# Kernel optimization log

Measured on AMD Instinct MI355X. Metric: run time of the kernel, lower is better.

Reference implementation:

```python
import jax, jax.numpy as jnp
import numpy as np

B, P, D, H, DH = 2, 2048, 1024, 16, 64
EPS = 1e-5

def layernorm(x, g, b):
    mu = jnp.mean(x, axis=-1, keepdims=True)
    var = jnp.mean((x - mu) ** 2, axis=-1, keepdims=True)
    return (x - mu) * jax.lax.rsqrt(var + EPS) * g + b

def setup_inputs() -> dict:
    key = jax.random.key(0)
    ks = jax.random.split(key, 16)
    s = lambda *sh: 1.0 / np.sqrt(sh[-2] if len(sh) > 1 else sh[-1])
    return {
        "x": jax.random.normal(ks[0], (B, P, D), jnp.float32),
        "Wq": jax.random.normal(ks[1], (H, D, DH), jnp.float32) / np.sqrt(D),
        "Wk": jax.random.normal(ks[2], (H, D, DH), jnp.float32) / np.sqrt(D),
        "Wv": jax.random.normal(ks[3], (H, D, DH), jnp.float32) / np.sqrt(D),
        "Wp": jax.random.normal(ks[4], (D, D), jnp.float32) / np.sqrt(D),
        "bp": jax.random.normal(ks[5], (D,), jnp.float32) * 0.01,
        "W1": jax.random.normal(ks[6], (D, 4 * D), jnp.float32) / np.sqrt(D),
        "b1": jax.random.normal(ks[7], (4 * D,), jnp.float32) * 0.01,
        "W2": jax.random.normal(ks[8], (4 * D, D), jnp.float32) / np.sqrt(4 * D),
        "b2": jax.random.normal(ks[9], (D,), jnp.float32) * 0.01,
        "g1": jnp.ones((D,), jnp.float32),
        "be1": jnp.zeros((D,), jnp.float32),
        "g2": jnp.ones((D,), jnp.float32),
        "be2": jnp.zeros((D,), jnp.float32),
    }

def reference(x, Wq, Wk, Wv, Wp, bp, W1, b1, W2, b2, g1, be1, g2, be2):
    Bb, Pp, Dd = x.shape
    h = layernorm(x, g1, be1)
    # per-head projections, stacked: [B,H,P,DH]
    q = jnp.einsum('bpd,hde->bhpe', h, Wq)
    k = jnp.einsum('bpd,hde->bhpe', h, Wk)
    v = jnp.einsum('bpd,hde->bhpe', h, Wv)
    # NOTE: source scales by dim_embd**-0.5 (C = x.shape[-1]), not dim_head
    scores = jnp.einsum('bhpe,bhqe->bhpq', q, k) * (Dd ** -0.5)
    mask = jnp.tril(jnp.ones((Pp, Pp), bool))
    scores = jnp.where(mask, scores, -jnp.inf)
    att = jax.nn.softmax(scores, axis=-1)
    o = jnp.einsum('bhpq,bhqe->bhpe', att, v)
    # concat heads: [B,P,H*DH]
    o = o.transpose(0, 2, 1, 3).reshape(Bb, Pp, -1)
    x = x + o @ Wp + bp
    h2 = layernorm(x, g2, be2)
    m = jax.nn.gelu(h2 @ W1 + b1, approximate=False)
    x = x + m @ W2 + b2
    return x
```

## Files before the change

### kernel.cpp

```cpp
#include <hip/hip_runtime.h>
#include <hip/hip_bf16.h>
#include <stdint.h>

typedef unsigned short u16;
typedef __attribute__((ext_vector_type(4))) float f32x4;
typedef __attribute__((ext_vector_type(8))) short bf16x8;
typedef __attribute__((ext_vector_type(4))) short bf16x4;
typedef __attribute__((ext_vector_type(4))) unsigned short u16x4;

static __device__ __forceinline__ u16 f2bf(float f) {
    union { float f; unsigned u; } v; v.f = f;
    unsigned r = v.u + 0x7fffu + ((v.u >> 16) & 1u);
    return (u16)(r >> 16);
}

static __device__ __forceinline__ void gload_lds16(const u16* g, u16* l) {
    __builtin_amdgcn_global_load_lds(
        (const __attribute__((address_space(1))) void*)(uintptr_t)g,
        (__attribute__((address_space(3))) void*)(uint32_t)(uintptr_t)l,
        16, 0, 0);
}

__global__ __launch_bounds__(256) void transpose_cast_b(
    const float* __restrict__ W, u16* __restrict__ out,
    int K, int N, long in_bs, long out_bs)
{
    __shared__ float tile[32][33];
    const float* Wb = W + (size_t)blockIdx.z * in_bs;
    u16* ob = out + (size_t)blockIdx.z * out_bs;
    int nt = blockIdx.x * 32, kt = blockIdx.y * 32;
    int tx = threadIdx.x & 31, ty = threadIdx.x >> 5;
    #pragma unroll
    for (int i = ty; i < 32; i += 8)
        tile[i][tx] = Wb[(size_t)(kt + i) * N + nt + tx];
    __syncthreads();
    #pragma unroll
    for (int i = ty; i < 32; i += 8)
        ob[(size_t)(nt + i) * K + kt + tx] = f2bf(tile[tx][i]);
}

__global__ __launch_bounds__(256) void ln_kernel(
    const float* __restrict__ x, const float* __restrict__ g,
    const float* __restrict__ be, u16* __restrict__ out)
{
    int row = blockIdx.x;
    int t = threadIdx.x;
    const float4* xr = (const float4*)(x + (size_t)row * 1024);
    float4 v = xr[t];
    float s = v.x + v.y + v.z + v.w;
    float sq = v.x * v.x + v.y * v.y + v.z * v.z + v.w * v.w;
    #pragma unroll
    for (int o = 1; o < 64; o <<= 1) {
        s  += __shfl_xor(s, o);
        sq += __shfl_xor(sq, o);
    }
    __shared__ float ps[4], pq[4];
    if ((t & 63) == 0) { ps[t >> 6] = s; pq[t >> 6] = sq; }
    __syncthreads();
    float S = ps[0] + ps[1] + ps[2] + ps[3];
    float Q = pq[0] + pq[1] + pq[2] + pq[3];
    float mu = S * (1.0f / 1024.0f);
    float var = Q * (1.0f / 1024.0f) - mu * mu;
    float rs = rsqrtf(var + 1e-5f);
    const float4 g4  = ((const float4*)g)[t];
    const float4 be4 = ((const float4*)be)[t];
    u16x4 o4;
    o4[0] = f2bf((v.x - mu) * rs * g4.x + be4.x);
    o4[1] = f2bf((v.y - mu) * rs * g4.y + be4.y);
    o4[2] = f2bf((v.z - mu) * rs * g4.z + be4.z);
    o4[3] = f2bf((v.w - mu) * rs * g4.w + be4.w);
    *(u16x4*)(out + (size_t)row * 1024 + t * 4) = o4;
}

template<int EPI>
__global__ __launch_bounds__(256) void gemm_bt(
    const u16* __restrict__ A, const u16* __restrict__ Bt,
    int M, int N, int K,
    const float* __restrict__ bias,
    void* __restrict__ Cout, u16* __restrict__ Kf, u16* __restrict__ Vf)
{
    __shared__ __align__(16) u16 SH[32768];
    const int tm = blockIdx.y * 128, tn = blockIdx.x * 128;
    const int t = threadIdx.x;
    const int lane = t & 63, wave = t >> 6;
    const int wr = wave >> 1, wc = wave & 1;
    const int lq = lane & 15, lg = lane >> 4;
    f32x4 acc[4][4] = {};

    const int srow8 = lane >> 3;
    const int skoff = ((lane & 7) ^ srow8) * 8;
    const u16* ag = A  + (size_t)(tm + wave * 32 + srow8) * K + skoff;
    const u16* bg = Bt + (size_t)(tn + wave * 32 + srow8) * K + skoff;

    auto STAGE = [&](int buf, int k0) {
        u16* ab = SH + buf * 16384 + wave * 2048;
        u16* bb = SH + buf * 16384 + 8192 + wave * 2048;
        #pragma unroll
        for (int j = 0; j < 4; ++j) {
            gload_lds16(ag + (size_t)(j * 8) * K + k0, ab + j * 512);
            gload_lds16(bg + (size_t)(j * 8) * K + k0, bb + j * 512);
        }
    };

    const int KT = K >> 6;
    STAGE(0, 0);
    STAGE(1, 64);
    asm volatile("s_waitcnt vmcnt(8)" ::: "memory");
    __builtin_amdgcn_sched_barrier(0);
    __builtin_amdgcn_s_barrier();

    for (int kt = 0; kt < KT; ++kt) {
        const int buf = kt & 1;
        const u16* abuf = SH + buf * 16384;
        const u16* bbuf = abuf + 8192;
        bf16x8 af[4][2], bfv[4][2];
        #pragma unroll
        for (int m = 0; m < 4; ++m) {
            const int row = wr * 64 + m * 16 + lq;
            #pragma unroll
            for (int kk = 0; kk < 2; ++kk) {
                const int slot = (kk * 4 + lg) ^ (row & 7);
                af[m][kk] = *(const bf16x8*)(abuf + row * 64 + slot * 8);
            }
        }
        #pragma unroll
        for (int n = 0; n < 4; ++n) {
            const int col = wc * 64 + n * 16 + lq;
            #pragma unroll
            for (int kk = 0; kk < 2; ++kk) {
                const int slot = (kk * 4 + lg) ^ (col & 7);
                bfv[n][kk] = *(const bf16x8*)(bbuf + col * 64 + slot * 8);
            }
        }
        asm volatile("s_waitcnt lgkmcnt(0)" ::: "memory");
        __builtin_amdgcn_sched_barrier(0);
        __builtin_amdgcn_s_barrier();

        const bool pre = (kt + 2 < KT);
        if (pre) STAGE(buf, (kt + 2) << 6);

        __builtin_amdgcn_s_setprio(1);
        #pragma unroll
        for (int m = 0; m < 4; ++m)
            #pragma unroll
            for (int n = 0; n < 4; ++n)
                #pragma unroll
                for (int kk = 0; kk < 2; ++kk)
                    acc[m][n] = __builtin_amdgcn_mfma_f32_16x16x32_bf16(
                        af[m][kk], bfv[n][kk], acc[m][n], 0, 0, 0);
        __builtin_amdgcn_s_setprio(0);

        if (kt + 1 < KT) {
            if (pre) asm volatile("s_waitcnt vmcnt(8)" ::: "memory");
            else     asm volatile("s_waitcnt vmcnt(0)" ::: "memory");
            __builtin_amdgcn_sched_barrier(0);
            __builtin_amdgcn_s_barrier();
        }
    }

    if (EPI == 2 || (EPI == 3 && tn < 1024)) {
        __syncthreads();
        #pragma unroll
        for (int n = 0; n < 4; ++n) {
            const int cl = wc * 64 + n * 16 + lq;
            #pragma unroll
            for (int m = 0; m < 4; ++m) {
                const int rl = wr * 64 + m * 16 + lg * 4;
                #pragma unroll
                for (int r = 0; r < 4; ++r) {
                    float v = acc[m][n][r];
                    if (EPI == 2) {
                        float xx = v + bias[tn + cl];
                        v = 0.5f * xx * (1.0f + erff(xx * 0.70710678118654752f));
                    }
                    SH[(rl + r) * 136 + cl] = f2bf(v);
                }
            }
        }
        __syncthreads();
        const int row = t >> 1, half = t & 1;
        const int ncols = (EPI == 2) ? N : 1024;
        const uint4* srow4 = (const uint4*)(SH + row * 136 + half * 64);
        uint4* drow = (uint4*)((u16*)Cout + (size_t)(tm + row) * ncols + tn + half * 64);
        #pragma unroll
        for (int i = 0; i < 8; ++i)
            drow[i] = srow4[i];
    } else if (EPI == 3) {
        __syncthreads();
        const bool isK = (tn < 2048);
        #pragma unroll
        for (int n = 0; n < 4; ++n) {
            const int cl = wc * 64 + n * 16 + lq;
            const int d = cl & 63, hl = cl >> 6;
            #pragma unroll
            for (int m = 0; m < 4; ++m) {
                const int rl0 = wr * 64 + m * 16 + lg * 4;
                #pragma unroll
                for (int r = 0; r < 4; ++r) {
                    const int rl = rl0 + r;
                    const int p = rl & 63, kl = rl >> 6;
                    int off;
                    if (isK)
                        off = ((p >> 4) * 2 + (d >> 5)) * 512 + ((d >> 3) & 3) * 128
                            + (p & 15) * 8 + (d & 7);
                    else
                        off = ((p >> 4) * 4 + (d >> 4)) * 256 + ((p >> 2) & 3) * 64
                            + (d & 15) * 4 + (p & 3);
                    SH[(hl * 2 + kl) * 4096 + off] = f2bf(acc[m][n][r]);
                }
            }
        }
        __syncthreads();
        const int img = t >> 6, ln = t & 63;
        const int hl = img >> 1, kl = img & 1;
        const int hh = ((tn - (isK ? 1024 : 2048)) >> 6) + hl;
        const int bb = tm >> 11, pp = tm & 2047;
        u16* base = (isK ? Kf : Vf) + (size_t)(bb * 16 + hh) * 131072
                  + (size_t)((pp >> 6) + kl) * 4096;
        const u16* simg = SH + img * 4096;
        #pragma unroll
        for (int i = 0; i < 8; ++i)
            *(uint4*)(base + ln * 8 + i * 512) = *(const uint4*)(simg + ln * 8 + i * 512);
    }
}

__global__ __launch_bounds__(256) void gemm_bt64(
    const u16* __restrict__ A, const u16* __restrict__ Bt,
    int M, int N, int K,
    const float* __restrict__ bias, const float* __restrict__ res,
    float* __restrict__ Cout)
{
    __shared__ __align__(16) u16 As[128 * 32];
    __shared__ __align__(16) u16 Bs[64 * 32];
    const int tm = blockIdx.y * 128, tn = blockIdx.x * 64;
    const int t = threadIdx.x;
    const int lane = t & 63, wave = t >> 6;
    const int wr = wave >> 1, wc = wave & 1;
    const int lq = lane & 15, lg = lane >> 4;
    f32x4 acc[4][2] = {};
    const int srow  = wave * 32 + (lane >> 2);
    const int srowB = wave * 16 + (lane >> 2);
    const int scol = (lane & 3) * 8;
    const u16* ag = A  + (size_t)(tm + srow)  * K + scol;
    const u16* bg = Bt + (size_t)(tn + srowB) * K + scol;
    u16* asl = As + wave * 1024;
    u16* bsl = Bs + wave * 512;
    const size_t rowskip = (size_t)16 * K;
    for (int k0 = 0; k0 < K; k0 += 32) {
        gload_lds16(ag + k0,           asl);
        gload_lds16(ag + k0 + rowskip, asl + 512);
        gload_lds16(bg + k0,           bsl);
        __syncthreads();
        bf16x8 af[4], bfr[2];
        #pragma unroll
        for (int m = 0; m < 4; ++m)
            af[m] = *(const bf16x8*)(As + (wr * 64 + m * 16 + lq) * 32 + lg * 8);
        #pragma unroll
        for (int n = 0; n < 2; ++n)
            bfr[n] = *(const bf16x8*)(Bs + (wc * 32 + n * 16 + lq) * 32 + lg * 8);
        #pragma unroll
        for (int m = 0; m < 4; ++m)
            #pragma unroll
            for (int n = 0; n < 2; ++n)
                acc[m][n] = __builtin_amdgcn_mfma_f32_16x16x32_bf16(af[m], bfr[n], acc[m][n], 0, 0, 0);
        __syncthreads();
    }
    #pragma unroll
    for (int m = 0; m < 4; ++m)
        #pragma unroll
        for (int n = 0; n < 2; ++n) {
            const int col = tn + wc * 32 + n * 16 + lq;
            #pragma unroll
            for (int r = 0; r < 4; ++r) {
                const int row = tm + wr * 64 + m * 16 + lg * 4 + r;
                Cout[(size_t)row * N + col] = acc[m][n][r] + bias[col] + res[(size_t)row * N + col];
            }
        }
}

__global__ __launch_bounds__(256, 4) void attn_kernel(
    const u16* __restrict__ qb, const u16* __restrict__ Kf,
    const u16* __restrict__ Vf, u16* __restrict__ o)
{
    const int P = 2048;
    __shared__ __align__(16) u16 KB[2][4096];
    __shared__ __align__(16) u16 VB[2][4096];
    int blk = blockIdx.x;
    int qt = 31 - (blk >> 5);
    int bh = blk & 31;
    int h = bh & 15, b = bh >> 4;
    int w = threadIdx.x >> 6, lane = threadIdx.x & 63;
    int lq = lane & 15, lg = lane >> 4;
    int q0 = qt * 64 + w * 16;
    const u16* qptr = qb + (size_t)(b * P + q0 + lq) * 1024 + h * 64 + lg * 8;
    bf16x8 qf0 = *(const bf16x8*)qptr;
    bf16x8 qf1 = *(const bf16x8*)(qptr + 32);
    const u16* Kfb = Kf + (size_t)bh * 131072;
    const u16* Vfb = Vf + (size_t)bh * 131072;
    const float C2 = 0.03125f * 1.44269504f;
    const int moff = w * 16 + lq;
    float m2 = -1e30f, l_run = 0.f;
    f32x4 accO[4] = {};
    const int nkvb = qt + 1;

    const int vsel = w >> 1, half = w & 1;
    auto STAGE = [&](int buf, int kvb) {
        const u16* src = (vsel ? Vfb : Kfb) + (size_t)kvb * 4096 + half * 2048 + lane * 8;
        u16* dst = (vsel ? &VB[buf][half * 2048] : &KB[buf][half * 2048]);
        #pragma unroll
        for (int i = 0; i < 4; ++i)
            gload_lds16(src + i * 512, dst + i * 512);
    };

    auto COMPUTE = [&](int buf, bool last) {
        const u16* kbase = KB[buf] + lane * 8;
        f32x4 st[4];
        #pragma unroll
        for (int ss = 0; ss < 4; ++ss) {
            bf16x8 kf0 = *(const bf16x8*)(kbase + ss * 1024);
            bf16x8 kf1 = *(const bf16x8*)(kbase + ss * 1024 + 512);
            f32x4 z = {0.f, 0.f, 0.f, 0.f};
            st[ss] = __builtin_amdgcn_mfma_f32_16x16x32_bf16(kf0, qf0, z, 0, 0, 0);
            st[ss] = __builtin_amdgcn_mfma_f32_16x16x32_bf16(kf1, qf1, st[ss], 0, 0, 0);
        }
        float rmax = -1e30f;
        #pragma unroll
        for (int ss = 0; ss < 4; ++ss)
            #pragma unroll
            for (int r = 0; r < 4; ++r) {
                float v = st[ss][r] * C2;
                if (last && (ss * 16 + lg * 4 + r > moff)) v = -1e30f;
                st[ss][r] = v;
                rmax = fmaxf(rmax, v);
            }
        rmax = fmaxf(rmax, __shfl_xor(rmax, 16));
        rmax = fmaxf(rmax, __shfl_xor(rmax, 32));
        if (__any(rmax > m2 + 11.5f)) {
            float m2n = fmaxf(m2, rmax);
            float alpha = exp2f(m2 - m2n);
            l_run *= alpha;
            #pragma unroll
            for (int r = 0; r < 4; ++r) {
                float ar = __shfl(alpha, lg * 4 + r);
                accO[0][r] *= ar; accO[1][r] *= ar; accO[2][r] *= ar; accO[3][r] *= ar;
            }
            m2 = m2n;
        }
        float psum = 0.f;
        bf16x4 pf[4];
        #pragma unroll
        for (int ss = 0; ss < 4; ++ss)
            #pragma unroll
            for (int r = 0; r < 4; ++r) {
                float pv = exp2f(st[ss][r] - m2);
                psum += pv;
                pf[ss][r] = (short)f2bf(pv);
            }
        psum += __shfl_xor(psum, 16);
        psum += __shfl_xor(psum, 32);
        l_run += psum;
        const u16* vbase = VB[buf] + lane * 4;
        #pragma unroll
        for (int ks = 0; ks < 4; ++ks)
            #pragma unroll
            for (int c = 0; c < 4; ++c) {
                bf16x4 vfr = *(const bf16x4*)(vbase + (ks * 4 + c) * 256);
                accO[c] = __builtin_amdgcn_mfma_f32_16x16x16bf16_1k(pf[ks], vfr, accO[c], 0, 0, 0);
            }
    };

    STAGE(0, 0);
    __syncthreads();
    int cur = 0;
    for (int kvb = 0; kvb < nkvb; ++kvb) {
        if (kvb + 1 < nkvb) STAGE(cur ^ 1, kvb + 1);
        COMPUTE(cur, kvb == nkvb - 1);
        __syncthreads();
        cur ^= 1;
    }

    #pragma unroll
    for (int r = 0; r < 4; ++r) {
        float l_r = __shfl(l_run, lg * 4 + r);
        float inv = 1.0f / l_r;
        size_t orow = (size_t)(b * P + q0 + lg * 4 + r) * 1024 + h * 64;
        #pragma unroll
        for (int c = 0; c < 4; ++c)
            o[orow + c * 16 + lq] = f2bf(accO[c][r] * inv);
    }
}

extern "C" void kernel_launch(void* const* d_in, const int* in_sizes, int n_in,
                              void* d_out, int out_size, void* d_ws, size_t ws_size,
                              hipStream_t stream)
{
    const float* x   = (const float*)d_in[0];
    const float* Wq  = (const float*)d_in[1];
    const float* Wk  = (const float*)d_in[2];
    const float* Wv  = (const float*)d_in[3];
    const float* Wp  = (const float*)d_in[4];
    const float* bp  = (const float*)d_in[5];
    const float* W1  = (const float*)d_in[6];
    const float* b1  = (const float*)d_in[7];
    const float* W2  = (const float*)d_in[8];
    const float* b2  = (const float*)d_in[9];
    const float* g1  = (const float*)d_in[10];
    const float* be1 = (const float*)d_in[11];
    const float* g2  = (const float*)d_in[12];
    const float* be2 = (const float*)d_in[13];

    char* ws = (char*)d_ws;
    u16*  h     = (u16*)(ws + 0);
    u16*  qbuf  = (u16*)(ws + 8388608);
    u16*  Kf    = (u16*)(ws + 16777216);
    u16*  Vf    = (u16*)(ws + 25165824);
    u16*  o     = (u16*)(ws + 33554432);
    float* x1   = (float*)(ws + 41943040);
    u16*  wqkvT = (u16*)(ws + 58720256);
    u16*  wpT   = (u16*)(ws + 65011712);
    u16*  w1T   = (u16*)(ws + 67108864);
    u16*  w2T   = (u16*)(ws + 75497472);
    u16*  m     = (u16*)(ws + 0);
    u16*  h2    = o;
    float* out  = (float*)d_out;

    transpose_cast_b<<<dim3(2, 32, 16), 256, 0, stream>>>(Wq, wqkvT,           1024, 64, 65536, 65536);
    transpose_cast_b<<<dim3(2, 32, 16), 256, 0, stream>>>(Wk, wqkvT + 1048576, 1024, 64, 65536, 65536);
    transpose_cast_b<<<dim3(2, 32, 16), 256, 0, stream>>>(Wv, wqkvT + 2097152, 1024, 64, 65536, 65536);
    transpose_cast_b<<<dim3(32, 32, 1), 256, 0, stream>>>(Wp, wpT, 1024, 1024, 0, 0);
    transpose_cast_b<<<dim3(128, 32, 1), 256, 0, stream>>>(W1, w1T, 1024, 4096, 0, 0);
    transpose_cast_b<<<dim3(32, 128, 1), 256, 0, stream>>>(W2, w2T, 4096, 1024, 0, 0);

    ln_kernel<<<4096, 256, 0, stream>>>(x, g1, be1, h);
    gemm_bt<3><<<dim3(24, 32), 256, 0, stream>>>(h, wqkvT, 4096, 3072, 1024, nullptr, qbuf, Kf, Vf);
    attn_kernel<<<1024, 256, 0, stream>>>(qbuf, Kf, Vf, o);
    gemm_bt64<<<dim3(16, 32), 256, 0, stream>>>(o, wpT, 4096, 1024, 1024, bp, x, x1);
    ln_kernel<<<4096, 256, 0, stream>>>(x1, g2, be2, h2);
    gemm_bt<2><<<dim3(32, 32), 256, 0, stream>>>(h2, w1T, 4096, 4096, 1024, b1, m, nullptr, nullptr);
    gemm_bt64<<<dim3(16, 32), 256, 0, stream>>>(m, w2T, 4096, 1024, 4096, b2, x1, out);
}
```

Before: 275.3 us.

## Halve GEMM K-tile to cut shared memory and raise occupancy

```diff
diff --git a/kernel.cpp b/kernel.cpp
--- a/kernel.cpp
+++ b/kernel.cpp
@@ -73,13 +73,13 @@
 }
 
 template<int EPI>
-__global__ __launch_bounds__(256) void gemm_bt(
+__global__ __launch_bounds__(256, 4) void gemm_bt(
     const u16* __restrict__ A, const u16* __restrict__ Bt,
     int M, int N, int K,
     const float* __restrict__ bias,
     void* __restrict__ Cout, u16* __restrict__ Kf, u16* __restrict__ Vf)
 {
-    __shared__ __align__(16) u16 SH[32768];
+    __shared__ __align__(16) u16 SH[16384];
     const int tm = blockIdx.y * 128, tn = blockIdx.x * 128;
     const int t = threadIdx.x;
     const int lane = t & 63, wave = t >> 6;
@@ -87,71 +87,63 @@
     const int lq = lane & 15, lg = lane >> 4;
     f32x4 acc[4][4] = {};
 
-    const int srow8 = lane >> 3;
-    const int skoff = ((lane & 7) ^ srow8) * 8;
-    const u16* ag = A  + (size_t)(tm + wave * 32 + srow8) * K + skoff;
-    const u16* bg = Bt + (size_t)(tn + wave * 32 + srow8) * K + skoff;
+    const int srow = lane >> 2;
+    const int sslot = ((lane & 3) ^ (srow & 3)) * 8;
+    const u16* ag = A  + (size_t)(tm + wave * 32 + srow) * K + sslot;
+    const u16* bg = Bt + (size_t)(tn + wave * 32 + srow) * K + sslot;
 
     auto STAGE = [&](int buf, int k0) {
-        u16* ab = SH + buf * 16384 + wave * 2048;
-        u16* bb = SH + buf * 16384 + 8192 + wave * 2048;
-        #pragma unroll
-        for (int j = 0; j < 4; ++j) {
-            gload_lds16(ag + (size_t)(j * 8) * K + k0, ab + j * 512);
-            gload_lds16(bg + (size_t)(j * 8) * K + k0, bb + j * 512);
+        u16* ab = SH + buf * 8192 + wave * 1024;
+        u16* bb = SH + buf * 8192 + 4096 + wave * 1024;
+        #pragma unroll
+        for (int j = 0; j < 2; ++j) {
+            gload_lds16(ag + (size_t)(j * 16) * K + k0, ab + j * 512);
+            gload_lds16(bg + (size_t)(j * 16) * K + k0, bb + j * 512);
         }
     };
 
-    const int KT = K >> 6;
+    const int KT = K >> 5;
     STAGE(0, 0);
-    STAGE(1, 64);
-    asm volatile("s_waitcnt vmcnt(8)" ::: "memory");
+    STAGE(1, 32);
+    asm volatile("s_waitcnt vmcnt(4)" ::: "memory");
     __builtin_amdgcn_sched_barrier(0);
     __builtin_amdgcn_s_barrier();
 
     for (int kt = 0; kt < KT; ++kt) {
         const int buf = kt & 1;
-        const u16* abuf = SH + buf * 16384;
-        const u16* bbuf = abuf + 8192;
-        bf16x8 af[4][2], bfv[4][2];
+        const u16* abuf = SH + buf * 8192;
+        const u16* bbuf = abuf + 4096;
+        bf16x8 af[4], bfv[4];
         #pragma unroll
         for (int m = 0; m < 4; ++m) {
             const int row = wr * 64 + m * 16 + lq;
-            #pragma unroll
-            for (int kk = 0; kk < 2; ++kk) {
-                const int slot = (kk * 4 + lg) ^ (row & 7);
-                af[m][kk] = *(const bf16x8*)(abuf + row * 64 + slot * 8);
-            }
+            const int slot = lg ^ (row & 3);
+            af[m] = *(const bf16x8*)(abuf + row * 32 + slot * 8);
         }
         #pragma unroll
         for (int n = 0; n < 4; ++n) {
             const int col = wc * 64 + n * 16 + lq;
-            #pragma unroll
-            for (int kk = 0; kk < 2; ++kk) {
-                const int slot = (kk * 4 + lg) ^ (col & 7);
-                bfv[n][kk] = *(const bf16x8*)(bbuf + col * 64 + slot * 8);
-            }
+            const int slot = lg ^ (col & 3);
+            bfv[n] = *(const bf16x8*)(bbuf + col * 32 + slot * 8);
         }
         asm volatile("s_waitcnt lgkmcnt(0)" ::: "memory");
         __builtin_amdgcn_sched_barrier(0);
         __builtin_amdgcn_s_barrier();
 
         const bool pre = (kt + 2 < KT);
-        if (pre) STAGE(buf, (kt + 2) << 6);
+        if (pre) STAGE(buf, (kt + 2) << 5);
 
         __builtin_amdgcn_s_setprio(1);
         #pragma unroll
         for (int m = 0; m < 4; ++m)
             #pragma unroll
             for (int n = 0; n < 4; ++n)
-                #pragma unroll
-                for (int kk = 0; kk < 2; ++kk)
-                    acc[m][n] = __builtin_amdgcn_mfma_f32_16x16x32_bf16(
-                        af[m][kk], bfv[n][kk], acc[m][n], 0, 0, 0);
+                acc[m][n] = __builtin_amdgcn_mfma_f32_16x16x32_bf16(
+                    af[m], bfv[n], acc[m][n], 0, 0, 0);
         __builtin_amdgcn_s_setprio(0);
 
         if (kt + 1 < KT) {
-            if (pre) asm volatile("s_waitcnt vmcnt(8)" ::: "memory");
+            if (pre) asm volatile("s_waitcnt vmcnt(4)" ::: "memory");
             else     asm volatile("s_waitcnt vmcnt(0)" ::: "memory");
             __builtin_amdgcn_sched_barrier(0);
             __builtin_amdgcn_s_barrier();
@@ -160,31 +152,38 @@
 
     if (EPI == 2 || (EPI == 3 && tn < 1024)) {
         __syncthreads();
-        #pragma unroll
-        for (int n = 0; n < 4; ++n) {
-            const int cl = wc * 64 + n * 16 + lq;
-            #pragma unroll
-            for (int m = 0; m < 4; ++m) {
-                const int rl = wr * 64 + m * 16 + lg * 4;
+        const int ncols = (EPI == 2) ? N : 1024;
+        #pragma unroll
+        for (int rh = 0; rh < 2; ++rh) {
+            if (rh) __syncthreads();
+            if (wr == rh) {
                 #pragma unroll
-                for (int r = 0; r < 4; ++r) {
-                    float v = acc[m][n][r];
-                    if (EPI == 2) {
-                        float xx = v + bias[tn + cl];
-                        v = 0.5f * xx * (1.0f + erff(xx * 0.70710678118654752f));
+                for (int n = 0; n < 4; ++n) {
+                    const int cl = wc * 64 + n * 16 + lq;
+                    #pragma unroll
+                    for (int m = 0; m < 4; ++m) {
+                        const int rl = m * 16 + lg * 4;
+                        #pragma unroll
+                        for (int r = 0; r < 4; ++r) {
+                            float v = acc[m][n][r];
+                            if (EPI == 2) {
+                                float xx = v + bias[tn + cl];
+                                v = 0.5f * xx * (1.0f + erff(xx * 0.70710678118654752f));
+                            }
+                            SH[(rl + r) * 136 + cl] = f2bf(v);
+                        }
                     }
-                    SH[(rl + r) * 136 + cl] = f2bf(v);
                 }
             }
-        }
-        __syncthreads();
-        const int row = t >> 1, half = t & 1;
-        const int ncols = (EPI == 2) ? N : 1024;
-        const uint4* srow4 = (const uint4*)(SH + row * 136 + half * 64);
-        uint4* drow = (uint4*)((u16*)Cout + (size_t)(tm + row) * ncols + tn + half * 64);
-        #pragma unroll
-        for (int i = 0; i < 8; ++i)
-            drow[i] = srow4[i];
+            __syncthreads();
+            const int row6 = t >> 2, q = t & 3;
+            #pragma unroll
+            for (int i = 0; i < 4; ++i) {
+                const uint4 vv = *(const uint4*)(SH + row6 * 136 + q * 32 + i * 8);
+                *(uint4*)((u16*)Cout + (size_t)(tm + rh * 64 + row6) * ncols
+                          + tn + q * 32 + i * 8) = vv;
+            }
+        }
     } else if (EPI == 3) {
         __syncthreads();
         const bool isK = (tn < 2048);
```

Measured after the change: 287.2 us. 4.3% more time.

## Double-buffer gemm_bt64 with BK=64, XOR-swizzled LDS and async prefetch

Applied to the files above, without the earlier changes.

```diff
diff --git a/kernel.cpp b/kernel.cpp
--- a/kernel.cpp
+++ b/kernel.cpp
@@ -230,41 +230,86 @@
     const float* __restrict__ bias, const float* __restrict__ res,
     float* __restrict__ Cout)
 {
-    __shared__ __align__(16) u16 As[128 * 32];
-    __shared__ __align__(16) u16 Bs[64 * 32];
+    __shared__ __align__(16) u16 SH[24576];
     const int tm = blockIdx.y * 128, tn = blockIdx.x * 64;
     const int t = threadIdx.x;
     const int lane = t & 63, wave = t >> 6;
     const int wr = wave >> 1, wc = wave & 1;
     const int lq = lane & 15, lg = lane >> 4;
     f32x4 acc[4][2] = {};
-    const int srow  = wave * 32 + (lane >> 2);
-    const int srowB = wave * 16 + (lane >> 2);
-    const int scol = (lane & 3) * 8;
-    const u16* ag = A  + (size_t)(tm + srow)  * K + scol;
-    const u16* bg = Bt + (size_t)(tn + srowB) * K + scol;
-    u16* asl = As + wave * 1024;
-    u16* bsl = Bs + wave * 512;
-    const size_t rowskip = (size_t)16 * K;
-    for (int k0 = 0; k0 < K; k0 += 32) {
-        gload_lds16(ag + k0,           asl);
-        gload_lds16(ag + k0 + rowskip, asl + 512);
-        gload_lds16(bg + k0,           bsl);
-        __syncthreads();
-        bf16x8 af[4], bfr[2];
+
+    const int srow8 = lane >> 3;
+    const int skoff = ((lane & 7) ^ srow8) * 8;
+    const u16* ag = A  + (size_t)(tm + wave * 32 + srow8) * K + skoff;
+    const u16* bg = Bt + (size_t)(tn + wave * 16 + srow8) * K + skoff;
+
+    auto STAGE = [&](int buf, int k0) {
+        u16* ab = SH + buf * 12288 + wave * 2048;
+        u16* bb = SH + buf * 12288 + 8192 + wave * 1024;
+        #pragma unroll
+        for (int j = 0; j < 4; ++j)
+            gload_lds16(ag + (size_t)(j * 8) * K + k0, ab + j * 512);
+        #pragma unroll
+        for (int j = 0; j < 2; ++j)
+            gload_lds16(bg + (size_t)(j * 8) * K + k0, bb + j * 512);
+    };
+
+    const int KT = K >> 6;
+    STAGE(0, 0);
+    STAGE(1, 64);
+    asm volatile("s_waitcnt vmcnt(6)" ::: "memory");
+    __builtin_amdgcn_sched_barrier(0);
+    __builtin_amdgcn_s_barrier();
+
+    for (int kt = 0; kt < KT; ++kt) {
+        const int buf = kt & 1;
+        const u16* abuf = SH + buf * 12288;
+        const u16* bbuf = abuf + 8192;
+        bf16x8 af[4][2], bfr[2][2];
+        #pragma unroll
+        for (int m = 0; m < 4; ++m) {
+            const int row = wr * 64 + m * 16 + lq;
+            #pragma unroll
+            for (int kk = 0; kk < 2; ++kk) {
+                const int slot = (kk * 4 + lg) ^ (row & 7);
+                af[m][kk] = *(const bf16x8*)(abuf + row * 64 + slot * 8);
+            }
+        }
+        #pragma unroll
+        for (int n = 0; n < 2; ++n) {
+            const int col = wc * 32 + n * 16 + lq;
+            #pragma unroll
+            for (int kk = 0; kk < 2; ++kk) {
+                const int slot = (kk * 4 + lg) ^ (col & 7);
+                bfr[n][kk] = *(const bf16x8*)(bbuf + col * 64 + slot * 8);
+            }
+        }
+        asm volatile("s_waitcnt lgkmcnt(0)" ::: "memory");
+        __builtin_amdgcn_sched_barrier(0);
+        __builtin_amdgcn_s_barrier();
+
+        const bool pre = (kt + 2 < KT);
+        if (pre) STAGE(buf, (kt + 2) << 6);
+
+        __builtin_amdgcn_s_setprio(1);
         #pragma unroll
         for (int m = 0; m < 4; ++m)
-            af[m] = *(const bf16x8*)(As + (wr * 64 + m * 16 + lq) * 32 + lg * 8);
-        #pragma unroll
-        for (int n = 0; n < 2; ++n)
-            bfr[n] = *(const bf16x8*)(Bs + (wc * 32 + n * 16 + lq) * 32 + lg * 8);
-        #pragma unroll
-        for (int m = 0; m < 4; ++m)
             #pragma unroll
             for (int n = 0; n < 2; ++n)
-                acc[m][n] = __builtin_amdgcn_mfma_f32_16x16x32_bf16(af[m], bfr[n], acc[m][n], 0, 0, 0);
-        __syncthreads();
-    }
+                #pragma unroll
+                for (int kk = 0; kk < 2; ++kk)
+                    acc[m][n] = __builtin_amdgcn_mfma_f32_16x16x32_bf16(
+                        af[m][kk], bfr[n][kk], acc[m][n], 0, 0, 0);
+        __builtin_amdgcn_s_setprio(0);
+
+        if (kt + 1 < KT) {
+            if (pre) asm volatile("s_waitcnt vmcnt(6)" ::: "memory");
+            else     asm volatile("s_waitcnt vmcnt(0)" ::: "memory");
+            __builtin_amdgcn_sched_barrier(0);
+            __builtin_amdgcn_s_barrier();
+        }
+    }
+
     #pragma unroll
     for (int m = 0; m < 4; ++m)
         #pragma unroll
```

Result: faster. 239.3 us (-13.1%).
